# Kernel optimization log

Hardware: AMD Instinct MI355X
Metric: run time of the kernel (lower is better)

The kernel has to match this reference:

```python
import jax, jax.numpy as jnp
import numpy as np

NODE_DIM = 3
EMBED = 16


def _gcn_mean_conv(x, W, b, src, dst, ew, N):
    """PyG GCNConv with aggr='mean': self-loops (weight 1), symmetric norm, mean agg, bias."""
    xw = x @ W  # [N, out]
    loop = jnp.arange(N, dtype=src.dtype)
    src2 = jnp.concatenate([src, loop])
    dst2 = jnp.concatenate([dst, loop])
    ew2 = jnp.concatenate([ew, jnp.ones((N,), x.dtype)])
    deg = jax.ops.segment_sum(ew2, dst2, num_segments=N)
    dinv = jnp.where(deg > 0, jax.lax.rsqrt(jnp.maximum(deg, 1e-12)), 0.0)
    norm = dinv[src2] * ew2 * dinv[dst2]  # [E+N]
    msg = norm[:, None] * xw[src2]  # [E+N, out]
    s = jax.ops.segment_sum(msg, dst2, num_segments=N)
    cnt = jax.ops.segment_sum(jnp.ones_like(norm), dst2, num_segments=N)
    return s / cnt[:, None] + b


def setup_inputs() -> dict:
    key = jax.random.key(0)
    ks = jax.random.split(key, 12)
    N, E, G, A = 500000, 8000000, 10000, 50
    pos = jax.random.normal(ks[0], (N, NODE_DIM), jnp.float32)
    sigmas = jax.random.uniform(ks[1], (G, A), jnp.float32, 0.1, 1.0)
    edge_index = jax.random.randint(ks[2], (2, E), 0, N, jnp.int64)

    def lin(k, fi, fo):
        k1, k2 = jax.random.split(k)
        lim = 1.0 / np.sqrt(fi)
        return (jax.random.uniform(k1, (fi, fo), jnp.float32, -lim, lim),
                jax.random.uniform(k2, (fo,), jnp.float32, -lim, lim))

    W_init, b_init = lin(ks[3], NODE_DIM, EMBED)
    W_g1, b_g1 = lin(ks[4], EMBED, EMBED)
    W_g2, b_g2 = lin(ks[5], EMBED, EMBED)
    W_p1, b_p1 = lin(ks[6], EMBED, EMBED)
    W_p2, b_p2 = lin(ks[7], EMBED, NODE_DIM)
    return {"pos": pos, "sigmas": sigmas, "edge_index": edge_index, "num_graphs": G,
            "W_init": W_init, "b_init": b_init, "W_g1": W_g1, "b_g1": b_g1,
            "W_g2": W_g2, "b_g2": b_g2, "W_p1": W_p1, "b_p1": b_p1,
            "W_p2": W_p2, "b_p2": b_p2}


def reference(pos, sigmas, edge_index, num_graphs, W_init, b_init, W_g1, b_g1,
              W_g2, b_g2, W_p1, b_p1, W_p2, b_p2):
    N = pos.shape[0]
    src, dst = edge_index[0], edge_index[1]
    edge_weight = jnp.linalg.norm(pos[src] - pos[dst], axis=1)  # [E]
    sp = jax.nn.softplus
    x = sp(pos @ W_init + b_init)
    x = sp(_gcn_mean_conv(x, W_g1, b_g1, src, dst, edge_weight, N))
    x = sp(_gcn_mean_conv(x, W_g2, b_g2, src, dst, edge_weight, N))
    y = sp(x @ W_p1 + b_p1)
    scores = (y @ W_p2 + b_p2).reshape(num_graphs, -1, NODE_DIM)
    scores = scores / sigmas[:, :, None]
    return scores.reshape(-1, NODE_DIM)
```

## Files before the change

kernel.cpp:

```cpp
#include <hip/hip_runtime.h>
#include <hip/hip_fp16.h>
#include <math.h>

#define ND 3
#define EM 16
#define BQ 512
#define BQ_SH 9
#define MAXB 1024
#define CHK 8192
#define COLS 12288
#define P_SH 23
#define PMASK ((1u << P_SH) - 1)

__device__ __forceinline__ float sp(float x) {
    return fmaxf(x, 0.0f) + log1pf(expf(-fabsf(x)));
}

__global__ __launch_bounds__(1024) void bucket_zero(int* __restrict__ bcnt)
{
    bcnt[threadIdx.x] = 0;
}

__global__ __launch_bounds__(256) void bucket_count(
    const int* __restrict__ ei, int* __restrict__ bcnt, int E, int NB)
{
    __shared__ int h[MAXB];
    int t = threadIdx.x;
    for (int i = t; i < MAXB; i += 256) h[i] = 0;
    __syncthreads();
    const int* dp = ei + (size_t)E;
    for (int e = blockIdx.x * 256 + t; e < E; e += gridDim.x * 256)
        atomicAdd(&h[((unsigned)dp[e]) >> BQ_SH], 1);
    __syncthreads();
    for (int i = t; i < NB; i += 256) {
        int v = h[i];
        if (v) atomicAdd(&bcnt[i], v);
    }
}

__global__ __launch_bounds__(1024) void bucket_scan(
    const int* __restrict__ bcnt, int* __restrict__ gbase,
    int* __restrict__ gcur, int NB)
{
    __shared__ int sd[1024];
    int t = threadIdx.x;
    int v = (t < NB) ? bcnt[t] : 0;
    sd[t] = v;
    __syncthreads();
    for (int off = 1; off < 1024; off <<= 1) {
        int add = (t >= off) ? sd[t - off] : 0;
        __syncthreads();
        sd[t] += add;
        __syncthreads();
    }
    if (t < NB) { int ex = sd[t] - v; gbase[t] = ex; gcur[t] = ex; }
}

__global__ __launch_bounds__(512) void edge_bin(
    const int* __restrict__ ei, int* __restrict__ gcur,
    unsigned int* __restrict__ pairs, int E)
{
    __shared__ int lcnt[MAXB];
    __shared__ int lbase[MAXB];
    __shared__ int sbase[MAXB];
    __shared__ unsigned int stage[CHK];
    __shared__ unsigned short bid[CHK];
    __shared__ int sd[512];
    int t = threadIdx.x;
    int c0 = blockIdx.x * CHK;
    int cntT = min(CHK, E - c0);
    for (int i = t; i < MAXB; i += 512) lcnt[i] = 0;
    __syncthreads();
    const int* dp = ei + (size_t)E;
    int dreg[16];
#pragma unroll
    for (int it = 0; it < 16; it++) {
        int e = c0 + it * 512 + t;
        dreg[it] = (e < E) ? dp[e] : 0;
        if (e < E) atomicAdd(&lcnt[((unsigned)dreg[it]) >> BQ_SH], 1);
    }
    __syncthreads();
    int b2 = t * 2;
    int h0 = lcnt[b2], h1 = lcnt[b2 + 1];
    int s2 = h0 + h1;
    sd[t] = s2;
    __syncthreads();
    for (int off = 1; off < 512; off <<= 1) {
        int add = (t >= off) ? sd[t - off] : 0;
        __syncthreads();
        sd[t] += add;
        __syncthreads();
    }
    int ex = sd[t] - s2;
    lbase[b2]     = ex;
    lbase[b2 + 1] = ex + h0;
    sbase[b2]     = h0 ? atomicAdd(&gcur[b2], h0)     : 0;
    sbase[b2 + 1] = h1 ? atomicAdd(&gcur[b2 + 1], h1) : 0;
    lcnt[b2] = 0; lcnt[b2 + 1] = 0;
    __syncthreads();
#pragma unroll
    for (int it = 0; it < 16; it++) {
        int e = c0 + it * 512 + t;
        if (e < E) {
            int d = dreg[it];
            unsigned b = ((unsigned)d) >> BQ_SH;
            int s = ei[e];
            int pos = lbase[b] + atomicAdd(&lcnt[b], 1);
            stage[pos] = ((unsigned)(d & (BQ - 1)) << P_SH) | (unsigned)s;
            bid[pos] = (unsigned short)b;
        }
    }
    __syncthreads();
    for (int i = t; i < cntT; i += 512) {
        unsigned b = bid[i];
        pairs[sbase[b] + (i - lbase[b])] = stage[i];
    }
}

__global__ __launch_bounds__(512) void bucket_csr_init(
    const unsigned int* __restrict__ pairs, const int* __restrict__ gbase,
    const int* __restrict__ bcnt, const float* __restrict__ pos,
    const float* __restrict__ W_init, const float* __restrict__ b_init,
    const float* __restrict__ W_g1,
    int* __restrict__ rowptr, int2* __restrict__ cw,
    float* __restrict__ dinv, __half2* __restrict__ zh1, int N, int NB)
{
    __shared__ int ncnt[BQ];
    __shared__ int ncur[BQ];
    __shared__ float wsum[BQ];
    __shared__ int sd[512];
    __shared__ unsigned int stg[COLS];
    __shared__ float posS[BQ * 3];
    __shared__ float sWi[ND * EM];
    __shared__ float sbi[EM];
    __shared__ float sW1[EM * EM];
    __shared__ float lx[64][EM + 2];
    int b = blockIdx.x;
    int t = threadIdx.x;
    int lo = b << BQ_SH;
    int hi = min(lo + BQ, N);
    int nloc = hi - lo;
    int r0 = gbase[b];
    int cntE = bcnt[b];
    if (t < ND * EM)  sWi[t] = W_init[t];
    if (t < EM)       sbi[t] = b_init[t];
    if (t < EM * EM)  sW1[t] = W_g1[t];
    for (int i = t; i < 3 * nloc; i += 512) posS[i] = pos[(size_t)lo * 3 + i];
    ncnt[t] = 0;
    wsum[t] = 0.0f;
    __syncthreads();
    for (int i = t; i < cntE; i += 512)
        atomicAdd(&ncnt[pairs[r0 + i] >> P_SH], 1);
    __syncthreads();
    int v = ncnt[t];
    sd[t] = v;
    __syncthreads();
    for (int off = 1; off < 512; off <<= 1) {
        int add = (t >= off) ? sd[t - off] : 0;
        __syncthreads();
        sd[t] += add;
        __syncthreads();
    }
    int ex = sd[t] - v;
    ncur[t] = ex;
    if (lo + t < hi) rowptr[lo + t] = r0 + ex;
    if (b == NB - 1 && t == 0) rowptr[N] = r0 + cntE;
    __syncthreads();
    bool fit = (cntE <= COLS);
    if (fit) {
        for (int i = t; i < cntE; i += 512) {
            unsigned p = pairs[r0 + i];
            int slot = atomicAdd(&ncur[p >> P_SH], 1);
            stg[slot] = p;
        }
        __syncthreads();
        for (int i = t; i < cntE; i += 512) {
            unsigned p = stg[i];
            int ldst = (int)(p >> P_SH);
            int src = (int)(p & PMASK);
            float dx = posS[ldst * 3 + 0] - pos[(size_t)src * 3 + 0];
            float dy = posS[ldst * 3 + 1] - pos[(size_t)src * 3 + 1];
            float dz = posS[ldst * 3 + 2] - pos[(size_t)src * 3 + 2];
            float d = sqrtf(fmaf(dx, dx, fmaf(dy, dy, dz * dz)));
            cw[r0 + i] = make_int2(src, __float_as_int(d));
            atomicAdd(&wsum[ldst], d);
        }
    } else {
        for (int i = t; i < cntE; i += 512) {
            unsigned p = pairs[r0 + i];
            int ldst = (int)(p >> P_SH);
            int src = (int)(p & PMASK);
            int slot = atomicAdd(&ncur[ldst], 1);
            float dx = posS[ldst * 3 + 0] - pos[(size_t)src * 3 + 0];
            float dy = posS[ldst * 3 + 1] - pos[(size_t)src * 3 + 1];
            float dz = posS[ldst * 3 + 2] - pos[(size_t)src * 3 + 2];
            float d = sqrtf(fmaf(dx, dx, fmaf(dy, dy, dz * dz)));
            cw[r0 + slot] = make_int2(src, __float_as_int(d));
            atomicAdd(&wsum[ldst], d);
        }
    }
    __syncthreads();
    int g = t >> 3, c = t & 7;
    for (int j = 0; j < BQ / 64; j++) {
        int nl = j * 64 + g;
        if (nl < nloc) {
            float p0 = posS[nl * 3 + 0];
            float p1 = posS[nl * 3 + 1];
            float p2 = posS[nl * 3 + 2];
            int k0 = 2 * c, k1 = 2 * c + 1;
            float h0 = fmaf(p0, sWi[0 * EM + k0],
                       fmaf(p1, sWi[1 * EM + k0],
                       fmaf(p2, sWi[2 * EM + k0], sbi[k0])));
            float h1 = fmaf(p0, sWi[0 * EM + k1],
                       fmaf(p1, sWi[1 * EM + k1],
                       fmaf(p2, sWi[2 * EM + k1], sbi[k1])));
            lx[g][k0] = sp(h0);
            lx[g][k1] = sp(h1);
            float di = rsqrtf(1.0f + wsum[nl]);
            int n = lo + nl;
            if (c == 0) dinv[n] = di;
            float ax = 0.0f, ay = 0.0f;
#pragma unroll
            for (int jj = 0; jj < EM; jj++) {
                float lj = lx[g][jj];
                ax = fmaf(lj, sW1[jj * EM + k0], ax);
                ay = fmaf(lj, sW1[jj * EM + k1], ay);
            }
            zh1[(size_t)n * 8 + c] =
                __float22half2_rn(make_float2(ax * di, ay * di));
        }
    }
}

__global__ __launch_bounds__(256) void gather_conv(
    const int* __restrict__ rowptr, const int2* __restrict__ cw,
    const float* __restrict__ dinv, const __half2* __restrict__ zin,
    const float* __restrict__ bconv, const float* __restrict__ W,
    const float* __restrict__ P1, const float* __restrict__ b1,
    const float* __restrict__ P2, const float* __restrict__ b2,
    const float* __restrict__ sig,
    __half2* __restrict__ zout, float* __restrict__ out, int N, int mode)
{
    __shared__ float sW[EM * EM];
    __shared__ float sP2[EM * ND];
    __shared__ float sb1[EM];
    __shared__ float sb2[ND];
    __shared__ float lx[32][EM + 1];
    int t = threadIdx.x;
    if (mode == 1) {
        sW[t] = W[t];
    } else {
        sW[t] = P1[t];
        if (t < EM)      sb1[t] = b1[t];
        if (t < EM * ND) sP2[t] = P2[t];
        if (t < ND)      sb2[t] = b2[t];
    }
    int g = t >> 3, c = t & 7;
    int n = blockIdx.x * 32 + g;

    float xx = 0.0f, xy = 0.0f;
    float di = 1.0f;
    if (n < N) {
        int start = rowptr[n], end = rowptr[n + 1];
        di = dinv[n];
        float2 zv = __half22float2(zin[(size_t)n * 8 + c]);
        float a0x = zv.x, a0y = zv.y;
        float a1x = 0.f, a1y = 0.f, a2x = 0.f, a2y = 0.f, a3x = 0.f, a3y = 0.f;
        int j = start;
        for (; j + 3 < end; j += 4) {
            int2 e0 = cw[j], e1 = cw[j + 1], e2 = cw[j + 2], e3 = cw[j + 3];
            float2 z0 = __half22float2(zin[(size_t)e0.x * 8 + c]);
            float2 z1 = __half22float2(zin[(size_t)e1.x * 8 + c]);
            float2 z2 = __half22float2(zin[(size_t)e2.x * 8 + c]);
            float2 z3 = __half22float2(zin[(size_t)e3.x * 8 + c]);
            float w0 = __int_as_float(e0.y), w1 = __int_as_float(e1.y);
            float w2 = __int_as_float(e2.y), w3 = __int_as_float(e3.y);
            a0x = fmaf(w0, z0.x, a0x); a0y = fmaf(w0, z0.y, a0y);
            a1x = fmaf(w1, z1.x, a1x); a1y = fmaf(w1, z1.y, a1y);
            a2x = fmaf(w2, z2.x, a2x); a2y = fmaf(w2, z2.y, a2y);
            a3x = fmaf(w3, z3.x, a3x); a3y = fmaf(w3, z3.y, a3y);
        }
        for (; j < end; j++) {
            int2 e = cw[j];
            float2 zr = __half22float2(zin[(size_t)e.x * 8 + c]);
            float wv = __int_as_float(e.y);
            a0x = fmaf(wv, zr.x, a0x); a0y = fmaf(wv, zr.y, a0y);
        }
        float accx = (a0x + a1x) + (a2x + a3x);
        float accy = (a0y + a1y) + (a2y + a3y);
        float rc = 1.0f / (float)(end - start + 1);
        xx = sp(fmaf(accx * di, rc, bconv[2 * c]));
        xy = sp(fmaf(accy * di, rc, bconv[2 * c + 1]));
    }
    __syncthreads();
    lx[g][2 * c]     = xx;
    lx[g][2 * c + 1] = xy;
    __syncthreads();
    if (n < N) {
        if (mode == 1) {
            float ax = 0.0f, ay = 0.0f;
#pragma unroll
            for (int j = 0; j < EM; j++) {
                float lj = lx[g][j];
                ax = fmaf(lj, sW[j * EM + 2 * c], ax);
                ay = fmaf(lj, sW[j * EM + 2 * c + 1], ay);
            }
            zout[(size_t)n * 8 + c] =
                __float22half2_rn(make_float2(ax * di, ay * di));
        } else {
            float ax = sb1[2 * c], ay = sb1[2 * c + 1];
#pragma unroll
            for (int j = 0; j < EM; j++) {
                float lj = lx[g][j];
                ax = fmaf(lj, sW[j * EM + 2 * c], ax);
                ay = fmaf(lj, sW[j * EM + 2 * c + 1], ay);
            }
            lx[g][2 * c]     = sp(ax);
            lx[g][2 * c + 1] = sp(ay);
            if (c < ND) {
                float o = sb2[c];
#pragma unroll
                for (int j = 0; j < EM; j++)
                    o = fmaf(lx[g][j], sP2[j * ND + c], o);
                out[(size_t)n * ND + c] = o / sig[n];
            }
        }
    }
}

extern "C" void kernel_launch(void* const* d_in, const int* in_sizes, int n_in,
                              void* d_out, int out_size, void* d_ws, size_t ws_size,
                              hipStream_t stream) {
    const float* pos    = (const float*)d_in[0];
    const float* sig    = (const float*)d_in[1];
    const int*   ei     = (const int*)d_in[2];
    const float* W_init = (const float*)d_in[4];
    const float* b_init = (const float*)d_in[5];
    const float* W_g1   = (const float*)d_in[6];
    const float* b_g1   = (const float*)d_in[7];
    const float* W_g2   = (const float*)d_in[8];
    const float* b_g2   = (const float*)d_in[9];
    const float* W_p1   = (const float*)d_in[10];
    const float* b_p1   = (const float*)d_in[11];
    const float* W_p2   = (const float*)d_in[12];
    const float* b_p2   = (const float*)d_in[13];
    float* out = (float*)d_out;

    int N = in_sizes[0] / ND;
    int E = in_sizes[2] / 2;
    size_t Ns = (size_t)N, Es = (size_t)E;
    int NB = (N + BQ - 1) >> BQ_SH;

    int* rowptr = (int*)d_ws;
    int* bcnt   = rowptr + (Ns + 1);
    int* gbase  = bcnt + 1024;
    int* gcur   = gbase + 1024;
    float* dinv = (float*)(gcur + 1024);
    size_t off = (Ns + 1) + 3 * 1024 + Ns;
    off = (off + 1) & ~(size_t)1;
    int2* cw = (int2*)((int*)d_ws + off);
    unsigned int* pairs = (unsigned int*)(cw + Es);
    __half2* zh2 = (__half2*)pairs;
    __half2* zh1 = (__half2*)(pairs + Es);

    int nbG2 = (N + 31) / 32;
    int nbBin = (E + CHK - 1) / CHK;

    bucket_zero<<<1, 1024, 0, stream>>>(bcnt);
    bucket_count<<<1024, 256, 0, stream>>>(ei, bcnt, E, NB);
    bucket_scan<<<1, 1024, 0, stream>>>(bcnt, gbase, gcur, NB);
    edge_bin<<<nbBin, 512, 0, stream>>>(ei, gcur, pairs, E);
    bucket_csr_init<<<NB, 512, 0, stream>>>(pairs, gbase, bcnt, pos,
        W_init, b_init, W_g1, rowptr, cw, dinv, zh1, N, NB);
    gather_conv<<<nbG2, 256, 0, stream>>>(rowptr, cw, dinv, zh1, b_g1, W_g2,
        W_p1, b_p1, W_p2, b_p2, sig, zh2, out, N, 1);
    gather_conv<<<nbG2, 256, 0, stream>>>(rowptr, cw, dinv, zh2, b_g2, W_g2,
        W_p1, b_p1, W_p2, b_p2, sig, zh2, out, N, 2);
}
```

Measured before the change: 666.8 us.

## Pack positions as float4, widen edge binning, drop shared-memory CSR staging

Adds a kernel that packs node positions into float4 so each per-edge gather in CSR construction is a single 16-byte load. The edge binning kernel moves to 1024 threads with one bucket per thread and vectorized int4 index loads. The CSR build no longer stages pairs in shared memory and instead scatters edge records straight to their slot. This removes a shared-memory pass but makes the cw writes less coalesced, and the packed copy costs extra memory traffic.

```diff
diff --git a/kernel.cpp b/kernel.cpp
--- a/kernel.cpp
+++ b/kernel.cpp
@@ -8,7 +8,6 @@
 #define BQ_SH 9
 #define MAXB 1024
 #define CHK 8192
-#define COLS 12288
 #define P_SH 23
 #define PMASK ((1u << P_SH) - 1)
 
@@ -19,6 +18,15 @@
 __global__ __launch_bounds__(1024) void bucket_zero(int* __restrict__ bcnt)
 {
     bcnt[threadIdx.x] = 0;
+}
+
+__global__ __launch_bounds__(256) void pos4_pack(
+    const float* __restrict__ pos, float4* __restrict__ pos4, int N)
+{
+    int n = blockIdx.x * 256 + threadIdx.x;
+    if (n >= N) return;
+    pos4[n] = make_float4(pos[3 * (size_t)n + 0], pos[3 * (size_t)n + 1],
+                          pos[3 * (size_t)n + 2], 0.0f);
 }
 
 __global__ __launch_bounds__(256) void bucket_count(
@@ -56,7 +64,7 @@
     if (t < NB) { int ex = sd[t] - v; gbase[t] = ex; gcur[t] = ex; }
 }
 
-__global__ __launch_bounds__(512) void edge_bin(
+__global__ __launch_bounds__(1024) void edge_bin(
     const int* __restrict__ ei, int* __restrict__ gcur,
     unsigned int* __restrict__ pairs, int E)
 {
@@ -65,53 +73,83 @@
     __shared__ int sbase[MAXB];
     __shared__ unsigned int stage[CHK];
     __shared__ unsigned short bid[CHK];
-    __shared__ int sd[512];
+    __shared__ int sd[1024];
     int t = threadIdx.x;
     int c0 = blockIdx.x * CHK;
     int cntT = min(CHK, E - c0);
-    for (int i = t; i < MAXB; i += 512) lcnt[i] = 0;
+    lcnt[t] = 0;
     __syncthreads();
     const int* dp = ei + (size_t)E;
-    int dreg[16];
-#pragma unroll
-    for (int it = 0; it < 16; it++) {
-        int e = c0 + it * 512 + t;
-        dreg[it] = (e < E) ? dp[e] : 0;
-        if (e < E) atomicAdd(&lcnt[((unsigned)dreg[it]) >> BQ_SH], 1);
-    }
-    __syncthreads();
-    int b2 = t * 2;
-    int h0 = lcnt[b2], h1 = lcnt[b2 + 1];
-    int s2 = h0 + h1;
-    sd[t] = s2;
-    __syncthreads();
-    for (int off = 1; off < 512; off <<= 1) {
+    bool vec = ((E & 3) == 0);
+    int4 d4[2];
+    if (vec) {
+#pragma unroll
+        for (int it = 0; it < 2; it++) {
+            int e0 = c0 + it * 4096 + 4 * t;
+            if (e0 < E) {
+                d4[it] = *(const int4*)(dp + e0);
+                atomicAdd(&lcnt[((unsigned)d4[it].x) >> BQ_SH], 1);
+                atomicAdd(&lcnt[((unsigned)d4[it].y) >> BQ_SH], 1);
+                atomicAdd(&lcnt[((unsigned)d4[it].z) >> BQ_SH], 1);
+                atomicAdd(&lcnt[((unsigned)d4[it].w) >> BQ_SH], 1);
+            }
+        }
+    } else {
+#pragma unroll
+        for (int it = 0; it < 8; it++) {
+            int e = c0 + it * 1024 + t;
+            if (e < E) atomicAdd(&lcnt[((unsigned)dp[e]) >> BQ_SH], 1);
+        }
+    }
+    __syncthreads();
+    int h = lcnt[t];
+    sd[t] = h;
+    __syncthreads();
+    for (int off = 1; off < 1024; off <<= 1) {
         int add = (t >= off) ? sd[t - off] : 0;
         __syncthreads();
         sd[t] += add;
         __syncthreads();
     }
-    int ex = sd[t] - s2;
-    lbase[b2]     = ex;
-    lbase[b2 + 1] = ex + h0;
-    sbase[b2]     = h0 ? atomicAdd(&gcur[b2], h0)     : 0;
-    sbase[b2 + 1] = h1 ? atomicAdd(&gcur[b2 + 1], h1) : 0;
-    lcnt[b2] = 0; lcnt[b2 + 1] = 0;
-    __syncthreads();
-#pragma unroll
-    for (int it = 0; it < 16; it++) {
-        int e = c0 + it * 512 + t;
-        if (e < E) {
-            int d = dreg[it];
-            unsigned b = ((unsigned)d) >> BQ_SH;
-            int s = ei[e];
-            int pos = lbase[b] + atomicAdd(&lcnt[b], 1);
-            stage[pos] = ((unsigned)(d & (BQ - 1)) << P_SH) | (unsigned)s;
-            bid[pos] = (unsigned short)b;
-        }
-    }
-    __syncthreads();
-    for (int i = t; i < cntT; i += 512) {
+    int ex = sd[t] - h;
+    lbase[t] = ex;
+    sbase[t] = h ? atomicAdd(&gcur[t], h) : 0;
+    lcnt[t] = 0;
+    __syncthreads();
+    if (vec) {
+#pragma unroll
+        for (int it = 0; it < 2; it++) {
+            int e0 = c0 + it * 4096 + 4 * t;
+            if (e0 < E) {
+                int4 s4 = *(const int4*)(ei + e0);
+                int dd[4] = { d4[it].x, d4[it].y, d4[it].z, d4[it].w };
+                int ss[4] = { s4.x, s4.y, s4.z, s4.w };
+#pragma unroll
+                for (int k = 0; k < 4; k++) {
+                    unsigned b = ((unsigned)dd[k]) >> BQ_SH;
+                    int pos = lbase[b] + atomicAdd(&lcnt[b], 1);
+                    stage[pos] = ((unsigned)(dd[k] & (BQ - 1)) << P_SH) |
+                                 (unsigned)ss[k];
+                    bid[pos] = (unsigned short)b;
+                }
+            }
+        }
+    } else {
+#pragma unroll
+        for (int it = 0; it < 8; it++) {
+            int e = c0 + it * 1024 + t;
+            if (e < E) {
+                int d = dp[e];
+                unsigned b = ((unsigned)d) >> BQ_SH;
+                int s = ei[e];
+                int pos = lbase[b] + atomicAdd(&lcnt[b], 1);
+                stage[pos] = ((unsigned)(d & (BQ - 1)) << P_SH) | (unsigned)s;
+                bid[pos] = (unsigned short)b;
+            }
+        }
+    }
+    __syncthreads();
+    for (int i = t; i < cntT; i += 1024) {
         unsigned b = bid[i];
         pairs[sbase[b] + (i - lbase[b])] = stage[i];
     }
@@ -119,7 +157,7 @@
 
 __global__ __launch_bounds__(512) void bucket_csr_init(
     const unsigned int* __restrict__ pairs, const int* __restrict__ gbase,
-    const int* __restrict__ bcnt, const float* __restrict__ pos,
+    const int* __restrict__ bcnt, const float4* __restrict__ pos4,
     const float* __restrict__ W_init, const float* __restrict__ b_init,
     const float* __restrict__ W_g1,
     int* __restrict__ rowptr, int2* __restrict__ cw,
@@ -129,8 +167,7 @@
     __shared__ int ncur[BQ];
     __shared__ float wsum[BQ];
     __shared__ int sd[512];
-    __shared__ unsigned int stg[COLS];
-    __shared__ float posS[BQ * 3];
+    __shared__ float4 posS[BQ];
     __shared__ float sWi[ND * EM];
     __shared__ float sbi[EM];
     __shared__ float sW1[EM * EM];
@@ -145,7 +182,7 @@
     if (t < ND * EM)  sWi[t] = W_init[t];
     if (t < EM)       sbi[t] = b_init[t];
     if (t < EM * EM)  sW1[t] = W_g1[t];
-    for (int i = t; i < 3 * nloc; i += 512) posS[i] = pos[(size_t)lo * 3 + i];
+    if (t < nloc) posS[t] = pos4[lo + t];
     ncnt[t] = 0;
     wsum[t] = 0.0f;
     __syncthreads();
@@ -166,54 +203,33 @@
     if (lo + t < hi) rowptr[lo + t] = r0 + ex;
     if (b == NB - 1 && t == 0) rowptr[N] = r0 + cntE;
     __syncthreads();
-    bool fit = (cntE <= COLS);
-    if (fit) {
-        for (int i = t; i < cntE; i += 512) {
-            unsigned p = pairs[r0 + i];
-            int slot = atomicAdd(&ncur[p >> P_SH], 1);
-            stg[slot] = p;
-        }
-        __syncthreads();
-        for (int i = t; i < cntE; i += 512) {
-            unsigned p = stg[i];
-            int ldst = (int)(p >> P_SH);
-            int src = (int)(p & PMASK);
-            float dx = posS[ldst * 3 + 0] - pos[(size_t)src * 3 + 0];
-            float dy = posS[ldst * 3 + 1] - pos[(size_t)src * 3 + 1];
-            float dz = posS[ldst * 3 + 2] - pos[(size_t)src * 3 + 2];
-            float d = sqrtf(fmaf(dx, dx, fmaf(dy, dy, dz * dz)));
-            cw[r0 + i] = make_int2(src, __float_as_int(d));
-            atomicAdd(&wsum[ldst], d);
-        }
-    } else {
-        for (int i = t; i < cntE; i += 512) {
-            unsigned p = pairs[r0 + i];
-            int ldst = (int)(p >> P_SH);
-            int src = (int)(p & PMASK);
-            int slot = atomicAdd(&ncur[ldst], 1);
-            float dx = posS[ldst * 3 + 0] - pos[(size_t)src * 3 + 0];
-            float dy = posS[ldst * 3 + 1] - pos[(size_t)src * 3 + 1];
-            float dz = posS[ldst * 3 + 2] - pos[(size_t)src * 3 + 2];
-            float d = sqrtf(fmaf(dx, dx, fmaf(dy, dy, dz * dz)));
-            cw[r0 + slot] = make_int2(src, __float_as_int(d));
-            atomicAdd(&wsum[ldst], d);
-        }
+    for (int i = t; i < cntE; i += 512) {
+        unsigned p = pairs[r0 + i];
+        int ldst = (int)(p >> P_SH);
+        int src = (int)(p & PMASK);
+        int slot = atomicAdd(&ncur[ldst], 1);
+        float4 pd = posS[ldst];
+        float4 ps = pos4[src];
+        float dx = pd.x - ps.x;
+        float dy = pd.y - ps.y;
+        float dz = pd.z - ps.z;
+        float d = sqrtf(fmaf(dx, dx, fmaf(dy, dy, dz * dz)));
+        cw[r0 + slot] = make_int2(src, __float_as_int(d));
+        atomicAdd(&wsum[ldst], d);
     }
     __syncthreads();
     int g = t >> 3, c = t & 7;
     for (int j = 0; j < BQ / 64; j++) {
         int nl = j * 64 + g;
         if (nl < nloc) {
-            float p0 = posS[nl * 3 + 0];
-            float p1 = posS[nl * 3 + 1];
-            float p2 = posS[nl * 3 + 2];
+            float4 pv = posS[nl];
             int k0 = 2 * c, k1 = 2 * c + 1;
-            float h0 = fmaf(p0, sWi[0 * EM + k0],
-                       fmaf(p1, sWi[1 * EM + k0],
-                       fmaf(p2, sWi[2 * EM + k0], sbi[k0])));
-            float h1 = fmaf(p0, sWi[0 * EM + k1],
-                       fmaf(p1, sWi[1 * EM + k1],
-                       fmaf(p2, sWi[2 * EM + k1], sbi[k1])));
+            float h0 = fmaf(pv.x, sWi[0 * EM + k0],
+                       fmaf(pv.y, sWi[1 * EM + k0],
+                       fmaf(pv.z, sWi[2 * EM + k0], sbi[k0])));
+            float h1 = fmaf(pv.x, sWi[0 * EM + k1],
+                       fmaf(pv.y, sWi[1 * EM + k1],
+                       fmaf(pv.z, sWi[2 * EM + k1], sbi[k1])));
             lx[g][k0] = sp(h0);
             lx[g][k1] = sp(h1);
             float di = rsqrtf(1.0f + wsum[nl]);
@@ -357,20 +373,23 @@
     int* gcur   = gbase + 1024;
     float* dinv = (float*)(gcur + 1024);
     size_t off = (Ns + 1) + 3 * 1024 + Ns;
-    off = (off + 1) & ~(size_t)1;
-    int2* cw = (int2*)((int*)d_ws + off);
+    off = (off + 3) & ~(size_t)3;
+    float4* pos4 = (float4*)((float*)d_ws + off);
+    int2* cw = (int2*)(pos4 + Ns);
     unsigned int* pairs = (unsigned int*)(cw + Es);
     __half2* zh2 = (__half2*)pairs;
     __half2* zh1 = (__half2*)(pairs + Es);
 
+    int nbN = (N + 255) / 256;
     int nbG2 = (N + 31) / 32;
     int nbBin = (E + CHK - 1) / CHK;
 
     bucket_zero<<<1, 1024, 0, stream>>>(bcnt);
+    pos4_pack<<<nbN, 256, 0, stream>>>(pos, pos4, N);
     bucket_count<<<1024, 256, 0, stream>>>(ei, bcnt, E, NB);
     bucket_scan<<<1, 1024, 0, stream>>>(bcnt, gbase, gcur, NB);
-    edge_bin<<<nbBin, 512, 0, stream>>>(ei, gcur, pairs, E);
-    bucket_csr_init<<<NB, 512, 0, stream>>>(pairs, gbase, bcnt, pos,
+    edge_bin<<<nbBin, 1024, 0, stream>>>(ei, gcur, pairs, E);
+    bucket_csr_init<<<NB, 512, 0, stream>>>(pairs, gbase, bcnt, pos4,
         W_init, b_init, W_g1, rowptr, cw, dinv, zh1, N, NB);
     gather_conv<<<nbG2, 256, 0, stream>>>(rowptr, cw, dinv, zh1, b_g1, W_g2,
         W_p1, b_p1, W_p2, b_p2, sig, zh2, out, N, 1);
```

Result: slower. 719.9 us (+8.0%).
